# Performance work log

Measured on AMD Instinct MI355X. Metric: run time of the kernel, lower is better.

Reference implementation:

```python
import jax, jax.numpy as jnp
import numpy as np

N = 262144      # total points
B = 128         # scenes (batch segments), 2048 points each
C_IN, C_MID, C_OUT = 256, 256, 512
SIGMA_EPS = 1e-4

def setup_inputs() -> dict:
    key = jax.random.key(0)
    k1, k2, k3, k4, k5 = jax.random.split(key, 5)
    pos = jax.random.normal(k1, (N, 3), dtype=jnp.float32)
    feature = jax.random.normal(k2, (N, C_IN), dtype=jnp.float32)
    batch = jnp.repeat(jnp.arange(B, dtype=jnp.int64), N // B)  # sorted segment ids, no empty segments
    W1 = jax.random.normal(k3, (C_IN + 3, C_MID), dtype=jnp.float32) * 0.02
    b1 = jnp.zeros((C_MID,), dtype=jnp.float32)
    W2 = jax.random.normal(k4, (C_MID, C_OUT), dtype=jnp.float32) * 0.02
    b2 = jnp.zeros((C_OUT,), dtype=jnp.float32)
    noise = jax.random.normal(k5, (B, C_OUT // 2), dtype=jnp.float32)  # reparam eps
    return {"pos": pos, "feature": feature, "batch": batch,
            "W1": W1, "b1": b1, "W2": W2, "b2": b2, "noise": noise}

def reference(pos, feature, batch, W1, b1, W2, b2, noise):
    # scatter_mean: per-scene centroid  [B,3]
    counts = jax.ops.segment_sum(jnp.ones((pos.shape[0],), pos.dtype), batch, num_segments=B)
    pos_center = jax.ops.segment_sum(pos, batch, num_segments=B) / counts[:, None]
    # PointConv with edges (i -> batch[i]): relative position gather
    rel = pos - pos_center[batch]                                  # [N,3]
    msg = jnp.concatenate([feature, rel], axis=1) @ W1 + b1        # [N, C_MID]
    msg = jax.nn.relu(msg)
    agg = jax.ops.segment_max(msg, batch, num_segments=B)          # [B, C_MID] (PointNetConv max aggr)
    out = agg @ W2 + b2                                            # [B, C_OUT]
    mu, sigma_raw = jnp.split(out, 2, axis=1)                      # [B,256] each
    sigma = jax.nn.softplus(sigma_raw) + SIGMA_EPS                 # to_sigma
    z_what_coarse = mu + sigma * noise                             # rsample
    return z_what_coarse
```

## Files before the change

### kernel.cpp

```cpp
#include <hip/hip_runtime.h>
#include <hip/hip_bf16.h>
#include <math.h>

#define PTS_PER 2048

typedef __attribute__((ext_vector_type(8))) short bf16x8;
typedef __attribute__((ext_vector_type(4))) float f32x4;

__device__ __forceinline__ unsigned int pk_bf16(float a, float b) {
    union { __hip_bfloat162 h; unsigned int u; } cv;
    cv.h = __float22bfloat162_rn(make_float2(a, b));
    return cv.u;
}
__device__ __forceinline__ unsigned short f2bf(float f) {
    union { __hip_bfloat16 h; unsigned short u; } cv;
    cv.h = __float2bfloat16(f);
    return cv.u;
}

__global__ __launch_bounds__(256) void prep_kernel(
    const float* __restrict__ pos, const float* __restrict__ W1,
    float* __restrict__ center, unsigned short* __restrict__ w1s) {
    int bid = blockIdx.x, t = threadIdx.x;
    if (bid < 128) {
        __shared__ float red[3 * 256];
        float sx = 0.f, sy = 0.f, sz = 0.f;
        int base = bid * PTS_PER;
        #pragma unroll
        for (int j = 0; j < 8; ++j) {
            int idx = base + j * 256 + t;
            sx += pos[idx * 3 + 0];
            sy += pos[idx * 3 + 1];
            sz += pos[idx * 3 + 2];
        }
        red[t] = sx; red[256 + t] = sy; red[512 + t] = sz;
        __syncthreads();
        for (int s = 128; s > 0; s >>= 1) {
            if (t < s) {
                red[t]       += red[t + s];
                red[256 + t] += red[256 + t + s];
                red[512 + t] += red[512 + t + s];
            }
            __syncthreads();
        }
        if (t == 0) {
            center[bid * 3 + 0] = red[0]   * (1.f / PTS_PER);
            center[bid * 3 + 1] = red[256] * (1.f / PTS_PER);
            center[bid * 3 + 2] = red[512] * (1.f / PTS_PER);
        }
    } else {
        int base = ((bid - 128) * 256 + t) * 4;
        int kk0 = base & 31;
        int rest = base >> 5;
        int n = rest & 255, ks = rest >> 8;
        #pragma unroll
        for (int j = 0; j < 4; ++j)
            w1s[base + j] = f2bf(W1[(ks * 32 + kk0 + j) * 256 + n]);
    }
}

__global__ __launch_bounds__(256, 3) void main_kernel(
    const float* __restrict__ feature, const float* __restrict__ pos,
    const float* __restrict__ W1, const float* __restrict__ center,
    const unsigned short* __restrict__ w1s, float* __restrict__ partial) {
    __shared__ unsigned short sA[64 * 264];
    __shared__ float sRel[64][3];

    int bid = blockIdx.x, t = threadIdx.x;
    int row0 = bid * 64;
    int scene = bid >> 5;

    if (t < 64) {
        int gr = row0 + t;
        sRel[t][0] = pos[gr * 3 + 0] - center[scene * 3 + 0];
        sRel[t][1] = pos[gr * 3 + 1] - center[scene * 3 + 1];
        sRel[t][2] = pos[gr * 3 + 2] - center[scene * 3 + 2];
    }

    int w = t >> 6, lane = t & 63, quad = lane >> 4, lo = lane & 15;

    bf16x8 bpre[4];
    #pragma unroll
    for (int ct = 0; ct < 4; ++ct) {
        int col = w * 64 + ct * 16 + lo;
        bpre[ct] = *(const bf16x8*)(w1s + col * 32 + quad * 8);
    }

    const float4* f4 = (const float4*)(feature + (size_t)row0 * 256);
    float4 av[16];
    #pragma unroll
    for (int it = 0; it < 16; ++it)
        av[it] = f4[it * 256 + t];
    #pragma unroll
    for (int it = 0; it < 16; ++it) {
        int fidx = it * 256 + t;
        int row = fidx >> 6, c4 = fidx & 63;
        uint2 h = make_uint2(pk_bf16(av[it].x, av[it].y),
                             pk_bf16(av[it].z, av[it].w));
        *(uint2*)(sA + row * 264 + c4 * 4) = h;
    }
    __syncthreads();

    f32x4 acc[4][4];
    #pragma unroll
    for (int rt = 0; rt < 4; ++rt)
        #pragma unroll
        for (int ct = 0; ct < 4; ++ct)
            acc[rt][ct] = (f32x4){0.f, 0.f, 0.f, 0.f};

    #pragma unroll
    for (int ks = 0; ks < 8; ++ks) {
        int kk = ks * 32 + quad * 8;
        bf16x8 afr[4], bfr[4];
        #pragma unroll
        for (int rt = 0; rt < 4; ++rt)
            afr[rt] = *(const bf16x8*)(sA + (rt * 16 + lo) * 264 + kk);
        #pragma unroll
        for (int ct = 0; ct < 4; ++ct) {
            int col = w * 64 + ct * 16 + lo;
            bfr[ct] = (ks == 0) ? bpre[ct]
                    : *(const bf16x8*)(w1s + (ks * 256 + col) * 32 + quad * 8);
        }
        #pragma unroll
        for (int rt = 0; rt < 4; ++rt)
            #pragma unroll
            for (int ct = 0; ct < 4; ++ct)
                acc[rt][ct] = __builtin_amdgcn_mfma_f32_16x16x32_bf16(
                    afr[rt], bfr[ct], acc[rt][ct], 0, 0, 0);
    }

    const float* Wp = W1 + 256 * 256;
    #pragma unroll
    for (int ct = 0; ct < 4; ++ct) {
        int col = w * 64 + ct * 16 + lo;
        float wp0 = Wp[col], wp1 = Wp[256 + col], wp2 = Wp[512 + col];
        float m = -3.4e38f;
        #pragma unroll
        for (int rt = 0; rt < 4; ++rt) {
            #pragma unroll
            for (int r = 0; r < 4; ++r) {
                int row = rt * 16 + quad * 4 + r;
                float v = acc[rt][ct][r] + sRel[row][0] * wp0
                        + sRel[row][1] * wp1 + sRel[row][2] * wp2;
                m = fmaxf(m, v);
            }
        }
        m = fmaxf(m, __shfl_xor(m, 16, 64));
        m = fmaxf(m, __shfl_xor(m, 32, 64));
        if (quad == 0)
            partial[(size_t)bid * 256 + col] = m;
    }
}

__global__ __launch_bounds__(256) void final_kernel(
    const float* __restrict__ partial, const float* __restrict__ b1,
    const float* __restrict__ W2, const float* __restrict__ b2,
    const float* __restrict__ noise, float* __restrict__ out) {
    int s = blockIdx.x, t = threadIdx.x;
    __shared__ float sa[256];
    const float* p = partial + (size_t)s * 32 * 256;
    float m = -3.4e38f;
    #pragma unroll
    for (int c = 0; c < 32; ++c)
        m = fmaxf(m, p[c * 256 + t]);
    sa[t] = fmaxf(m + b1[t], 0.f);
    __syncthreads();
    float mu = b2[t], sr = b2[256 + t];
    #pragma unroll 8
    for (int k = 0; k < 256; ++k) {
        float a = sa[k];
        mu += a * W2[k * 512 + t];
        sr += a * W2[k * 512 + 256 + t];
    }
    float sp = (sr > 20.f) ? sr : log1pf(expf(sr));
    float sigma = sp + 1e-4f;
    out[s * 256 + t] = mu + sigma * noise[s * 256 + t];
}

extern "C" void kernel_launch(void* const* d_in, const int* in_sizes, int n_in,
                              void* d_out, int out_size, void* d_ws, size_t ws_size,
                              hipStream_t stream) {
    const float* pos     = (const float*)d_in[0];
    const float* feature = (const float*)d_in[1];
    const float* W1      = (const float*)d_in[3];
    const float* b1      = (const float*)d_in[4];
    const float* W2      = (const float*)d_in[5];
    const float* b2      = (const float*)d_in[6];
    const float* noise   = (const float*)d_in[7];
    float* out = (float*)d_out;

    char* ws = (char*)d_ws;
    float* partial        = (float*)ws;
    unsigned short* w1s   = (unsigned short*)(ws + (4 << 20));
    float* center         = (float*)(ws + (4 << 20) + 131072);

    prep_kernel <<<192, 256, 0, stream>>>(pos, W1, center, w1s);
    main_kernel <<<4096, 256, 0, stream>>>(feature, pos, W1, center, w1s, partial);
    final_kernel<<<128, 256, 0, stream>>>(partial, b1, W2, b2, noise, out);
}
```

Baseline: 404.9 us.

## Defer centroid subtraction past segment max via linearity of position term

Result: no change. 409.0 us (+1.0%).

```diff
diff --git a/kernel.cpp b/kernel.cpp
--- a/kernel.cpp
+++ b/kernel.cpp
@@ -19,63 +19,28 @@
 }
 
 __global__ __launch_bounds__(256) void prep_kernel(
-    const float* __restrict__ pos, const float* __restrict__ W1,
-    float* __restrict__ center, unsigned short* __restrict__ w1s) {
-    int bid = blockIdx.x, t = threadIdx.x;
-    if (bid < 128) {
-        __shared__ float red[3 * 256];
-        float sx = 0.f, sy = 0.f, sz = 0.f;
-        int base = bid * PTS_PER;
-        #pragma unroll
-        for (int j = 0; j < 8; ++j) {
-            int idx = base + j * 256 + t;
-            sx += pos[idx * 3 + 0];
-            sy += pos[idx * 3 + 1];
-            sz += pos[idx * 3 + 2];
-        }
-        red[t] = sx; red[256 + t] = sy; red[512 + t] = sz;
-        __syncthreads();
-        for (int s = 128; s > 0; s >>= 1) {
-            if (t < s) {
-                red[t]       += red[t + s];
-                red[256 + t] += red[256 + t + s];
-                red[512 + t] += red[512 + t + s];
-            }
-            __syncthreads();
-        }
-        if (t == 0) {
-            center[bid * 3 + 0] = red[0]   * (1.f / PTS_PER);
-            center[bid * 3 + 1] = red[256] * (1.f / PTS_PER);
-            center[bid * 3 + 2] = red[512] * (1.f / PTS_PER);
-        }
-    } else {
-        int base = ((bid - 128) * 256 + t) * 4;
-        int kk0 = base & 31;
-        int rest = base >> 5;
-        int n = rest & 255, ks = rest >> 8;
-        #pragma unroll
-        for (int j = 0; j < 4; ++j)
-            w1s[base + j] = f2bf(W1[(ks * 32 + kk0 + j) * 256 + n]);
-    }
+    const float* __restrict__ W1, unsigned short* __restrict__ w1s) {
+    int base = (blockIdx.x * 256 + threadIdx.x) * 4;
+    int kk0 = base & 31;
+    int rest = base >> 5;
+    int n = rest & 255, ks = rest >> 8;
+    #pragma unroll
+    for (int j = 0; j < 4; ++j)
+        w1s[base + j] = f2bf(W1[(ks * 32 + kk0 + j) * 256 + n]);
 }
 
 __global__ __launch_bounds__(256, 3) void main_kernel(
     const float* __restrict__ feature, const float* __restrict__ pos,
-    const float* __restrict__ W1, const float* __restrict__ center,
+    const float* __restrict__ W1,
     const unsigned short* __restrict__ w1s, float* __restrict__ partial) {
     __shared__ unsigned short sA[64 * 264];
-    __shared__ float sRel[64][3];
+    __shared__ float sPos[64 * 3];
 
     int bid = blockIdx.x, t = threadIdx.x;
     int row0 = bid * 64;
-    int scene = bid >> 5;
 
-    if (t < 64) {
-        int gr = row0 + t;
-        sRel[t][0] = pos[gr * 3 + 0] - center[scene * 3 + 0];
-        sRel[t][1] = pos[gr * 3 + 1] - center[scene * 3 + 1];
-        sRel[t][2] = pos[gr * 3 + 2] - center[scene * 3 + 2];
-    }
+    if (t < 192)
+        sPos[t] = pos[row0 * 3 + t];
 
     int w = t >> 6, lane = t & 63, quad = lane >> 4, lo = lane & 15;
 
@@ -140,8 +105,8 @@
             #pragma unroll
             for (int r = 0; r < 4; ++r) {
                 int row = rt * 16 + quad * 4 + r;
-                float v = acc[rt][ct][r] + sRel[row][0] * wp0
-                        + sRel[row][1] * wp1 + sRel[row][2] * wp2;
+                float v = acc[rt][ct][r] + sPos[row * 3 + 0] * wp0
+                        + sPos[row * 3 + 1] * wp1 + sPos[row * 3 + 2] * wp2;
                 m = fmaxf(m, v);
             }
         }
@@ -153,18 +118,49 @@
 }
 
 __global__ __launch_bounds__(256) void final_kernel(
-    const float* __restrict__ partial, const float* __restrict__ b1,
+    const float* __restrict__ partial, const float* __restrict__ pos,
+    const float* __restrict__ W1, const float* __restrict__ b1,
     const float* __restrict__ W2, const float* __restrict__ b2,
     const float* __restrict__ noise, float* __restrict__ out) {
     int s = blockIdx.x, t = threadIdx.x;
+    __shared__ float red[3 * 256];
     __shared__ float sa[256];
+
     const float* p = partial + (size_t)s * 32 * 256;
     float m = -3.4e38f;
     #pragma unroll
     for (int c = 0; c < 32; ++c)
         m = fmaxf(m, p[c * 256 + t]);
-    sa[t] = fmaxf(m + b1[t], 0.f);
+
+    float sx = 0.f, sy = 0.f, sz = 0.f;
+    int base = s * PTS_PER;
+    #pragma unroll
+    for (int j = 0; j < 8; ++j) {
+        int idx = base + j * 256 + t;
+        sx += pos[idx * 3 + 0];
+        sy += pos[idx * 3 + 1];
+        sz += pos[idx * 3 + 2];
+    }
+    red[t] = sx; red[256 + t] = sy; red[512 + t] = sz;
     __syncthreads();
+    for (int st = 128; st > 0; st >>= 1) {
+        if (t < st) {
+            red[t]       += red[t + st];
+            red[256 + t] += red[256 + t + st];
+            red[512 + t] += red[512 + t + st];
+        }
+        __syncthreads();
+    }
+    float cx = red[0]   * (1.f / PTS_PER);
+    float cy = red[256] * (1.f / PTS_PER);
+    float cz = red[512] * (1.f / PTS_PER);
+
+    const float* Wp = W1 + 256 * 256;
+    float cwp = cx * Wp[t] + cy * Wp[256 + t] + cz * Wp[512 + t];
+
+    sa[t] = fmaxf(m - cwp + b1[t], 0.f);
+    __syncthreads();
+
     float mu = b2[t], sr = b2[256 + t];
     #pragma unroll 8
     for (int k = 0; k < 256; ++k) {
@@ -192,9 +188,8 @@
     char* ws = (char*)d_ws;
     float* partial        = (float*)ws;
     unsigned short* w1s   = (unsigned short*)(ws + (4 << 20));
-    float* center         = (float*)(ws + (4 << 20) + 131072);
 
-    prep_kernel <<<192, 256, 0, stream>>>(pos, W1, center, w1s);
-    main_kernel <<<4096, 256, 0, stream>>>(feature, pos, W1, center, w1s, partial);
-    final_kernel<<<128, 256, 0, stream>>>(partial, b1, W2, b2, noise, out);
+    prep_kernel <<<  64, 256, 0, stream>>>(W1, w1s);
+    main_kernel <<<4096, 256, 0, stream>>>(feature, pos, W1, w1s, partial);
+    final_kernel<<< 128, 256, 0, stream>>>(partial, pos, W1, b1, W2, b2, noise, out);
 }
```
